# Kernel optimization log

Measured on AMD Instinct MI355X. Metric: run time of the kernel, lower is better.

## Reference

```python
import jax, jax.numpy as jnp
import numpy as np

B, S, D, H = 2, 2048, 1024, 16
HW = D // H  # head width = 64
MASK_FILL = -100000000.0


def setup_inputs() -> dict:
    key0 = jax.random.key(0)
    ks = jax.random.split(key0, 12)
    inp = {
        "query": jax.random.normal(ks[0], (B, S, D), jnp.float32),
        "key": jax.random.normal(ks[1], (B, S, D), jnp.float32),
        "value": jax.random.normal(ks[2], (B, S, D), jnp.float32),
        # bool mask, True masks; broadcasts over batch and heads
        "mask": jax.random.randint(ks[3], (S, S), 0, 2).astype(jnp.bool_),
        # per-head projection kernels: (heads, head_width, d_in)
        "Wq": jax.random.normal(ks[4], (H, HW, D), jnp.float32) * 0.02,
        "bq": jnp.zeros((H, HW), jnp.float32),
        "Wk": jax.random.normal(ks[5], (H, HW, D), jnp.float32) * 0.02,
        "bk": jnp.zeros((H, HW), jnp.float32),
        "Wv": jax.random.normal(ks[6], (H, HW, D), jnp.float32) * 0.02,
        "bv": jnp.zeros((H, HW), jnp.float32),
        # collapse projector: contracts (heads, head_width) -> d_output
        "Wo": jax.random.normal(ks[7], (D, H, HW), jnp.float32) * 0.02,
        "bo": jnp.zeros((D,), jnp.float32),
    }
    return inp


def reference(query, key, value, mask, Wq, bq, Wk, bk, Wv, bv, Wo, bo):
    # head projections -> (b, h, s, w)
    q = jnp.einsum("bsd,hwd->bhsw", query, Wq) + bq[:, None, :]
    k = jnp.einsum("btd,hwd->bhtw", key, Wk) + bk[:, None, :]
    v = jnp.einsum("btd,hwd->bhtw", value, Wv) + bv[:, None, :]
    # unscaled logits, masked_fill, softmax (matches original exactly)
    logits = jnp.einsum("bhsw,bhtw->bhst", q, k)
    logits = jnp.where(mask, MASK_FILL, logits)
    score = jax.nn.softmax(logits, axis=-1)
    # NOTE: original divides AV output by sqrt(head_width) AFTER softmax
    attn = jnp.einsum("bhst,bhtw->bhsw", score, v) / jnp.sqrt(jnp.float32(HW))
    # collapse heads -> (b, s, d_output)
    out = jnp.einsum("bhsw,ohw->bso", attn, Wo) + bo
    return out
```

## Files before the change

### kernel.cpp

```cpp
#include <hip/hip_runtime.h>
#include <math.h>

#define S_LEN   2048
#define D_MODEL 1024
#define N_HEADS 16
#define HEAD_W  64
#define BATCH   2
#define MROWS   (BATCH * S_LEN)
#define MASK_FILL -100000000.0f
#define LOG2E 1.4426950408889634f

typedef __attribute__((ext_vector_type(8))) short bf16x8;
typedef __attribute__((ext_vector_type(4))) float f32x4;
typedef unsigned short u16;
typedef unsigned int   u32;
typedef unsigned long long u64;

__device__ __forceinline__ u16 f2bf(float f) {
    u32 u = __float_as_uint(f);
    return (u16)((u + 0x7fffu + ((u >> 16) & 1u)) >> 16);
}

__device__ __forceinline__ void gld_lds16(const void* gp, void* lp) {
    __builtin_amdgcn_global_load_lds(
        (const __attribute__((address_space(1))) u32*)gp,
        (__attribute__((address_space(3))) u32*)lp, 16, 0, 0);
}

__global__ __launch_bounds__(256) void mask_bits_kernel(
    const unsigned char* __restrict__ mask, u64* __restrict__ bits) {
    __shared__ int isByte;
    if (threadIdx.x == 0) isByte = 0;
    __syncthreads();
    const int e0 = blockIdx.x * 2048;
    const uint2 v = ((const uint2*)(mask + e0))[threadIdx.x];
    if (((v.x | v.y) & 0xFFFFFF00u) != 0u) isByte = 1;
    __syncthreads();
    const int ib = isByte;
    const int* mi = (const int*)mask;
#pragma unroll
    for (int j = 0; j < 8; ++j) {
        const int e = e0 + j * 256 + threadIdx.x;
        const bool m = ib ? (mask[e] != 0) : (mi[e] != 0);
        const u64 bl = __ballot(m);
        if ((e & 63) == 0) bits[e >> 6] = bl;
    }
}

struct CvtJobs {
    const float* src[7];
    u16* dst[7];
    int n[7];
};
__global__ void cvt_bf16_kernel(CvtJobs j) {
    const int t = blockIdx.y;
    const float* s = j.src[t];
    u16* d = j.dst[t];
    const int n = j.n[t];
    int i = (blockIdx.x * 256 + threadIdx.x) * 4;
    if (i < n) {
        float4 v = *(const float4*)(s + i);
        ushort4 o;
        o.x = f2bf(v.x); o.y = f2bf(v.y); o.z = f2bf(v.z); o.w = f2bf(v.w);
        *(ushort4*)(d + i) = o;
    }
}

__device__ __forceinline__ void gemm_core_bf16(const u16* __restrict__ A,
                                               const u16* __restrict__ Bt,
                                               int m0, int n0, f32x4 acc[4][4]) {
    __shared__ u16 As[2][4096];
    __shared__ u16 Bs[2][4096];
    const int tid = threadIdx.x;
    const int wv = tid >> 6, ln = tid & 63;
    const int lane16 = ln & 15, quad = ln >> 4;
    const int wr = (wv >> 1) * 64, wc = (wv & 1) * 64;
    const u16* A0 = A + (size_t)(m0 + ln) * D_MODEL + wv * 8;
    const u16* A1 = A + (size_t)(m0 + 64 + ln) * D_MODEL + wv * 8;
    const u16* B0 = Bt + (size_t)(n0 + ln) * D_MODEL + wv * 8;
    const u16* B1 = Bt + (size_t)(n0 + 64 + ln) * D_MODEL + wv * 8;

    gld_lds16(A0, &As[0][wv * 1024]);
    gld_lds16(A1, &As[0][wv * 1024 + 512]);
    gld_lds16(B0, &Bs[0][wv * 1024]);
    gld_lds16(B1, &Bs[0][wv * 1024 + 512]);

    for (int kt = 0; kt < D_MODEL / 32; ++kt) {
        const int buf = kt & 1;
        __syncthreads();
        if (kt < D_MODEL / 32 - 1) {
            const int ko = (kt + 1) * 32;
            gld_lds16(A0 + ko, &As[buf ^ 1][wv * 1024]);
            gld_lds16(A1 + ko, &As[buf ^ 1][wv * 1024 + 512]);
            gld_lds16(B0 + ko, &Bs[buf ^ 1][wv * 1024]);
            gld_lds16(B1 + ko, &Bs[buf ^ 1][wv * 1024 + 512]);
        }
        bf16x8 af[4], bfv[4];
#pragma unroll
        for (int mt = 0; mt < 4; ++mt)
            af[mt] = *(const bf16x8*)&As[buf][quad * 1024 + (wr + mt * 16 + lane16) * 8];
#pragma unroll
        for (int nt = 0; nt < 4; ++nt)
            bfv[nt] = *(const bf16x8*)&Bs[buf][quad * 1024 + (wc + nt * 16 + lane16) * 8];
#pragma unroll
        for (int mt = 0; mt < 4; ++mt)
#pragma unroll
            for (int nt = 0; nt < 4; ++nt)
                acc[mt][nt] = __builtin_amdgcn_mfma_f32_16x16x32_bf16(
                    af[mt], bfv[nt], acc[mt][nt], 0, 0, 0);
    }
}

__global__ __launch_bounds__(256, 2) void qkv_gemm_kernel(
    const u16* __restrict__ xq, const u16* __restrict__ xk, const u16* __restrict__ xv,
    const u16* __restrict__ wq, const u16* __restrict__ wk, const u16* __restrict__ wv,
    const float* __restrict__ bq, const float* __restrict__ bk, const float* __restrict__ bv,
    u16* __restrict__ qb, u16* __restrict__ kb, u16* __restrict__ vtmp) {
    const u16* A; const u16* Bt; const float* bias; u16* outp;
    const int z = blockIdx.z;
    if (z == 0)      { A = xq; Bt = wq; bias = bq; outp = qb; }
    else if (z == 1) { A = xk; Bt = wk; bias = bk; outp = kb; }
    else             { A = xv; Bt = wv; bias = bv; outp = vtmp; }
    f32x4 acc[4][4] = {};
    const int m0 = blockIdx.y * 128, n0 = blockIdx.x * 128;
    gemm_core_bf16(A, Bt, m0, n0, acc);

    const int tid = threadIdx.x;
    const int wvi = tid >> 6, ln = tid & 63;
    const int lane16 = ln & 15, quad = ln >> 4;
    const int wr = (wvi >> 1) * 64, wc = (wvi & 1) * 64;
    const float scale = (z == 0) ? LOG2E : 1.0f;
#pragma unroll
    for (int nt = 0; nt < 4; ++nt) {
        const int n = n0 + wc + nt * 16 + lane16;
        const float bb = bias[n];
        const int h = n >> 6, w = n & 63;
#pragma unroll
        for (int mt = 0; mt < 4; ++mt)
#pragma unroll
            for (int r = 0; r < 4; ++r) {
                const int m = m0 + wr + mt * 16 + quad * 4 + r;
                const int bidx = m >> 11, s = m & 2047;
                outp[((size_t)((bidx * N_HEADS + h) * S_LEN + s)) * HEAD_W + w] =
                    f2bf((acc[mt][nt][r] + bb) * scale);
            }
    }
}

__global__ __launch_bounds__(256) void vtrans_kernel(
    const u16* __restrict__ vtmp, u16* __restrict__ vbt) {
    __shared__ u16 T[64][72];
    const int tid = threadIdx.x;
    const int bh = blockIdx.y;
    const int s0 = blockIdx.x * 64;
    const int row = tid >> 2, seg = (tid & 3) * 16;
    const u16* src = vtmp + ((size_t)bh * S_LEN + s0 + row) * HEAD_W + seg;
    uint4 a = *(const uint4*)src;
    uint4 b2 = *(const uint4*)(src + 8);
    u16 tmp[16];
    *(uint4*)tmp = a; *(uint4*)(tmp + 8) = b2;
#pragma unroll
    for (int j = 0; j < 16; ++j) T[seg + j][row] = tmp[j];
    __syncthreads();
    u16* dst = vbt + ((size_t)bh * HEAD_W + row) * S_LEN + s0 + seg;
    *(uint4*)dst       = *(const uint4*)&T[row][seg];
    *(uint4*)(dst + 8) = *(const uint4*)&T[row][seg + 8];
}

__global__ __launch_bounds__(256, 2) void out_gemm_kernel(
    const u16* __restrict__ ab, const u16* __restrict__ wo,
    const float* __restrict__ bo, float* __restrict__ out) {
    f32x4 acc[4][4] = {};
    const int m0 = blockIdx.y * 128, n0 = blockIdx.x * 128;
    gemm_core_bf16(ab, wo, m0, n0, acc);
    const int tid = threadIdx.x;
    const int wvi = tid >> 6, ln = tid & 63;
    const int lane16 = ln & 15, quad = ln >> 4;
    const int wr = (wvi >> 1) * 64, wc = (wvi & 1) * 64;
#pragma unroll
    for (int nt = 0; nt < 4; ++nt) {
        const int n = n0 + wc + nt * 16 + lane16;
        const float bb = bo[n];
#pragma unroll
        for (int mt = 0; mt < 4; ++mt)
#pragma unroll
            for (int r = 0; r < 4; ++r) {
                const int m = m0 + wr + mt * 16 + quad * 4 + r;
                out[(size_t)m * D_MODEL + n] = acc[mt][nt][r] + bb;
            }
    }
}

__global__ __launch_bounds__(256, 2) void attn_kernel(
    const u16* __restrict__ qbuf, const u16* __restrict__ kbuf,
    const u16* __restrict__ vbt, const u64* __restrict__ mbits,
    float* __restrict__ Opart, float* __restrict__ lpart) {
    __shared__ u16 Ks[2][4096];
    __shared__ u16 Vt[2][4096];
    __shared__ u16 Ps[4][32 * 72];
    const int tid = threadIdx.x;
    const int wv = tid >> 6, ln = tid & 63;
    const int lane16 = ln & 15, quad = ln >> 4;
    const int s_blk = blockIdx.x * 128;
    const int h = blockIdx.y;
    const int b = blockIdx.z >> 1, hf = blockIdx.z & 1;
    const int c0 = hf * 16;
    const size_t hb = ((size_t)(b * N_HEADS + h)) * S_LEN * HEAD_W;
    const u16* Qg = qbuf + hb;
    const u16* Kg = kbuf + hb;
    const u16* Vg = vbt + hb;

    bf16x8 qa[2][2];
#pragma unroll
    for (int mt = 0; mt < 2; ++mt)
#pragma unroll
        for (int kk = 0; kk < 2; ++kk)
            qa[mt][kk] = *(const bf16x8*)(Qg +
                (size_t)(s_blk + wv * 32 + mt * 16 + lane16) * HEAD_W + kk * 32 + quad * 8);

    const size_t mrow0 = (size_t)(s_blk + wv * 32 + lane16) * 32;
    const size_t mrow1 = (size_t)(s_blk + wv * 32 + 16 + lane16) * 32;
    u64 mwCur0 = mbits[mrow0 + c0], mwCur1 = mbits[mrow1 + c0];
    u64 mwNx0 = 0, mwNx1 = 0;

    {
        const int t0g = c0 * 64;
        const int i0 = 2 * wv, i1 = 2 * wv + 1;
        gld_lds16(Kg + (size_t)(t0g + ln) * HEAD_W + i0 * 8, &Ks[0][i0 * 512]);
        gld_lds16(Kg + (size_t)(t0g + ln) * HEAD_W + i1 * 8, &Ks[0][i1 * 512]);
        gld_lds16(Vg + (size_t)ln * S_LEN + t0g + i0 * 8, &Vt[0][i0 * 512]);
        gld_lds16(Vg + (size_t)ln * S_LEN + t0g + i1 * 8, &Vt[0][i1 * 512]);
    }

    f32x4 oacc[2][4] = {};
    float lsum[2] = {0.0f, 0.0f};

    for (int ci = 0; ci < 16; ++ci) {
        const int c = c0 + ci;
        const int buf = ci & 1;
        __syncthreads();
        if (ci < 15) {
            const int t1 = (c + 1) * 64;
            const int i0 = 2 * wv, i1 = 2 * wv + 1;
            gld_lds16(Kg + (size_t)(t1 + ln) * HEAD_W + i0 * 8, &Ks[buf ^ 1][i0 * 512]);
            gld_lds16(Kg + (size_t)(t1 + ln) * HEAD_W + i1 * 8, &Ks[buf ^ 1][i1 * 512]);
            gld_lds16(Vg + (size_t)ln * S_LEN + t1 + i0 * 8, &Vt[buf ^ 1][i0 * 512]);
            gld_lds16(Vg + (size_t)ln * S_LEN + t1 + i1 * 8, &Vt[buf ^ 1][i1 * 512]);
            mwNx0 = mbits[mrow0 + c + 1];
            mwNx1 = mbits[mrow1 + c + 1];
        }

        f32x4 st[4][2] = {};
#pragma unroll
        for (int kk = 0; kk < 2; ++kk)
#pragma unroll
            for (int ntT = 0; ntT < 4; ++ntT) {
                bf16x8 kf = *(const bf16x8*)&Ks[buf][(kk * 4 + quad) * 512 + (ntT * 16 + lane16) * 8];
#pragma unroll
                for (int mt = 0; mt < 2; ++mt)
                    st[ntT][mt] = __builtin_amdgcn_mfma_f32_16x16x32_bf16(
                        kf, qa[mt][kk], st[ntT][mt], 0, 0, 0);
            }

#pragma unroll
        for (int mt = 0; mt < 2; ++mt) {
            const u64 mw = mt ? mwCur1 : mwCur0;
            float ls = 0.0f;
#pragma unroll
            for (int ntT = 0; ntT < 4; ++ntT) {
                const u32 nib = (u32)(mw >> (ntT * 16 + quad * 4)) & 15u;
                float p0 = exp2f(st[ntT][mt][0]); if (nib & 1u) p0 = 0.0f;
                float p1 = exp2f(st[ntT][mt][1]); if (nib & 2u) p1 = 0.0f;
                float p2 = exp2f(st[ntT][mt][2]); if (nib & 4u) p2 = 0.0f;
                float p3 = exp2f(st[ntT][mt][3]); if (nib & 8u) p3 = 0.0f;
                ls += (p0 + p1) + (p2 + p3);
                uint2 pk;
                pk.x = __builtin_amdgcn_perm(__float_as_uint(p1) + 0x8000u,
                                             __float_as_uint(p0) + 0x8000u, 0x07060302u);
                pk.y = __builtin_amdgcn_perm(__float_as_uint(p3) + 0x8000u,
                                             __float_as_uint(p2) + 0x8000u, 0x07060302u);
                *(uint2*)&Ps[wv][(mt * 16 + lane16) * 72 + ntT * 16 + quad * 4] = pk;
            }
            lsum[mt] += ls;
        }

        bf16x8 pf[2][2];
#pragma unroll
        for (int mt = 0; mt < 2; ++mt)
#pragma unroll
            for (int kk = 0; kk < 2; ++kk)
                pf[mt][kk] = *(const bf16x8*)&Ps[wv][(mt * 16 + lane16) * 72 + kk * 32 + quad * 8];
#pragma unroll
        for (int kk = 0; kk < 2; ++kk)
#pragma unroll
            for (int ntw = 0; ntw < 4; ++ntw) {
                bf16x8 vf = *(const bf16x8*)&Vt[buf][(kk * 4 + quad) * 512 + (ntw * 16 + lane16) * 8];
#pragma unroll
                for (int mt = 0; mt < 2; ++mt)
                    oacc[mt][ntw] = __builtin_amdgcn_mfma_f32_16x16x32_bf16(
                        pf[mt][kk], vf, oacc[mt][ntw], 0, 0, 0);
            }
        mwCur0 = mwNx0; mwCur1 = mwNx1;
    }

    float* OpB = Opart + ((size_t)(hf * 4096 + b * 2048)) * 1024;
#pragma unroll
    for (int mt = 0; mt < 2; ++mt) {
#pragma unroll
        for (int r = 0; r < 4; ++r) {
            const int s = s_blk + wv * 32 + mt * 16 + quad * 4 + r;
            float* dst = OpB + (size_t)s * 1024 + h * 64;
#pragma unroll
            for (int ntw = 0; ntw < 4; ++ntw)
                dst[ntw * 16 + lane16] = oacc[mt][ntw][r];
        }
        float lm = lsum[mt];
        lm += __shfl_xor(lm, 16);
        lm += __shfl_xor(lm, 32);
        if (quad == 0) {
            const int srow = s_blk + wv * 32 + mt * 16 + lane16;
            lpart[(size_t)(hf * 4096 + b * 2048 + srow) * 16 + h] = lm;
        }
    }
}

__global__ __launch_bounds__(256) void combine_kernel(
    const float* __restrict__ Op, const float* __restrict__ lp,
    u16* __restrict__ ab) {
    const int idx4 = blockIdx.x * 256 + threadIdx.x;
    const int row = idx4 >> 8;
    const int d = (idx4 & 255) * 4;
    const int h = d >> 6;
    const float l = lp[(size_t)row * 16 + h] + lp[(size_t)(4096 + row) * 16 + h];
    const float inv = 0.125f / l;
    float4 a = *(const float4*)(Op + (size_t)row * 1024 + d);
    float4 b = *(const float4*)(Op + (size_t)(4096 + row) * 1024 + d);
    ushort4 o;
    o.x = f2bf((a.x + b.x) * inv);
    o.y = f2bf((a.y + b.y) * inv);
    o.z = f2bf((a.z + b.z) * inv);
    o.w = f2bf((a.w + b.w) * inv);
    *(ushort4*)(ab + (size_t)row * 1024 + d) = o;
}

extern "C" void kernel_launch(void* const* d_in, const int* in_sizes, int n_in,
                              void* d_out, int out_size, void* d_ws, size_t ws_size,
                              hipStream_t stream) {
    const float* query = (const float*)d_in[0];
    const float* key   = (const float*)d_in[1];
    const float* value = (const float*)d_in[2];
    const void*  mask  = d_in[3];
    const float* Wq = (const float*)d_in[4];
    const float* bq = (const float*)d_in[5];
    const float* Wk = (const float*)d_in[6];
    const float* bk = (const float*)d_in[7];
    const float* Wv = (const float*)d_in[8];
    const float* bv = (const float*)d_in[9];
    const float* Wo = (const float*)d_in[10];
    const float* bo = (const float*)d_in[11];
    float* out = (float*)d_out;

    char* ws = (char*)d_ws;
    const size_t MB = 1024 * 1024;
    u64* bits = (u64*)ws;
    u16* wob  = (u16*)(ws + 1 * MB);
    u16* qb   = (u16*)(ws + 3 * MB);
    u16* kb   = (u16*)(ws + 11 * MB);
    u16* vbt  = (u16*)(ws + 19 * MB);
    char* uA = ws + 27 * MB;
    u16* xq   = (u16*)(uA);
    u16* xk   = (u16*)(uA + 8 * MB);
    u16* xv   = (u16*)(uA + 16 * MB);
    u16* wqb  = (u16*)(uA + 24 * MB);
    u16* wkb  = (u16*)(uA + 26 * MB);
    u16* wvb  = (u16*)(uA + 28 * MB);
    u16* vtmp = (u16*)(uA + 30 * MB);
    float* Opart = (float*)(uA);
    float* lpart = (float*)(uA + 32 * MB);
    u16* ab = qb;

    const size_t NACT = (size_t)MROWS * D_MODEL;
    const size_t NW   = (size_t)D_MODEL * D_MODEL;

    mask_bits_kernel<<<2048, 256, 0, stream>>>((const unsigned char*)mask, bits);

    CvtJobs j;
    j.src[0] = query; j.dst[0] = xq;  j.n[0] = (int)NACT;
    j.src[1] = key;   j.dst[1] = xk;  j.n[1] = (int)NACT;
    j.src[2] = value; j.dst[2] = xv;  j.n[2] = (int)NACT;
    j.src[3] = Wq;    j.dst[3] = wqb; j.n[3] = (int)NW;
    j.src[4] = Wk;    j.dst[4] = wkb; j.n[4] = (int)NW;
    j.src[5] = Wv;    j.dst[5] = wvb; j.n[5] = (int)NW;
    j.src[6] = Wo;    j.dst[6] = wob; j.n[6] = (int)NW;
    cvt_bf16_kernel<<<dim3(NACT / 1024, 7), 256, 0, stream>>>(j);

    qkv_gemm_kernel<<<dim3(D_MODEL / 128, MROWS / 128, 3), 256, 0, stream>>>(
        xq, xk, xv, wqb, wkb, wvb, bq, bk, bv, qb, kb, vtmp);
    vtrans_kernel<<<dim3(S_LEN / 64, BATCH * N_HEADS), 256, 0, stream>>>(vtmp, vbt);
    attn_kernel<<<dim3(S_LEN / 128, N_HEADS, BATCH * 2), 256, 0, stream>>>(
        qb, kb, vbt, bits, Opart, lpart);
    combine_kernel<<<4096, 256, 0, stream>>>(Opart, lpart, ab);
    out_gemm_kernel<<<dim3(D_MODEL / 128, MROWS / 128), 256, 0, stream>>>(
        ab, wob, bo, out);
}
```

Before: 313.8 us.

## Fuse mask-bit and bf16 conversion kernels, raise occupancy bounds, use intrinsic bf16 pack

```diff
diff --git a/kernel.cpp b/kernel.cpp
--- a/kernel.cpp
+++ b/kernel.cpp
@@ -1,4 +1,5 @@
 #include <hip/hip_runtime.h>
+#include <hip/hip_bf16.h>
 #include <math.h>
 
 #define S_LEN   2048
@@ -21,14 +22,41 @@
     return (u16)((u + 0x7fffu + ((u >> 16) & 1u)) >> 16);
 }
 
+__device__ __forceinline__ u32 pack_bf16x2(float lo, float hi) {
+    __hip_bfloat162 t = __float22bfloat162_rn(make_float2(lo, hi));
+    u32 r;
+    __builtin_memcpy(&r, &t, 4);
+    return r;
+}
+
 __device__ __forceinline__ void gld_lds16(const void* gp, void* lp) {
     __builtin_amdgcn_global_load_lds(
         (const __attribute__((address_space(1))) u32*)gp,
         (__attribute__((address_space(3))) u32*)lp, 16, 0, 0);
 }
 
-__global__ __launch_bounds__(256) void mask_bits_kernel(
-    const unsigned char* __restrict__ mask, u64* __restrict__ bits) {
+struct CvtJobs {
+    const float* src[7];
+    u16* dst[7];
+    int n[7];
+};
+__global__ __launch_bounds__(256) void prep_kernel(
+    CvtJobs j, const unsigned char* __restrict__ mask, u64* __restrict__ bits) {
+    const int t = blockIdx.y;
+    if (t < 7) {
+        const float* s = j.src[t];
+        u16* d = j.dst[t];
+        const int n = j.n[t];
+        int i = (blockIdx.x * 256 + threadIdx.x) * 4;
+        if (i < n) {
+            float4 v = *(const float4*)(s + i);
+            ushort4 o;
+            o.x = f2bf(v.x); o.y = f2bf(v.y); o.z = f2bf(v.z); o.w = f2bf(v.w);
+            *(ushort4*)(d + i) = o;
+        }
+        return;
+    }
+    if (blockIdx.x >= 2048) return;
     __shared__ int isByte;
     if (threadIdx.x == 0) isByte = 0;
     __syncthreads();
@@ -39,30 +67,11 @@
     const int ib = isByte;
     const int* mi = (const int*)mask;
 #pragma unroll
-    for (int j = 0; j < 8; ++j) {
-        const int e = e0 + j * 256 + threadIdx.x;
+    for (int jj = 0; jj < 8; ++jj) {
+        const int e = e0 + jj * 256 + threadIdx.x;
         const bool m = ib ? (mask[e] != 0) : (mi[e] != 0);
         const u64 bl = __ballot(m);
         if ((e & 63) == 0) bits[e >> 6] = bl;
-    }
-}
-
-struct CvtJobs {
-    const float* src[7];
-    u16* dst[7];
-    int n[7];
-};
-__global__ void cvt_bf16_kernel(CvtJobs j) {
-    const int t = blockIdx.y;
-    const float* s = j.src[t];
-    u16* d = j.dst[t];
-    const int n = j.n[t];
-    int i = (blockIdx.x * 256 + threadIdx.x) * 4;
-    if (i < n) {
-        float4 v = *(const float4*)(s + i);
-        ushort4 o;
-        o.x = f2bf(v.x); o.y = f2bf(v.y); o.z = f2bf(v.z); o.w = f2bf(v.w);
-        *(ushort4*)(d + i) = o;
     }
 }
 
@@ -111,7 +120,7 @@
     }
 }
 
-__global__ __launch_bounds__(256, 2) void qkv_gemm_kernel(
+__global__ __launch_bounds__(256, 4) void qkv_gemm_kernel(
     const u16* __restrict__ xq, const u16* __restrict__ xk, const u16* __restrict__ xv,
     const u16* __restrict__ wq, const u16* __restrict__ wk, const u16* __restrict__ wv,
     const float* __restrict__ bq, const float* __restrict__ bk, const float* __restrict__ bv,
@@ -167,7 +176,7 @@
     *(uint4*)(dst + 8) = *(const uint4*)&T[row][seg + 8];
 }
 
-__global__ __launch_bounds__(256, 2) void out_gemm_kernel(
+__global__ __launch_bounds__(256, 4) void out_gemm_kernel(
     const u16* __restrict__ ab, const u16* __restrict__ wo,
     const float* __restrict__ bo, float* __restrict__ out) {
     f32x4 acc[4][4] = {};
@@ -191,7 +200,7 @@
     }
 }
 
-__global__ __launch_bounds__(256, 2) void attn_kernel(
+__global__ __launch_bounds__(256, 3) void attn_kernel(
     const u16* __restrict__ qbuf, const u16* __restrict__ kbuf,
     const u16* __restrict__ vbt, const u64* __restrict__ mbits,
     float* __restrict__ Opart, float* __restrict__ lpart) {
@@ -265,7 +274,7 @@
 #pragma unroll
         for (int mt = 0; mt < 2; ++mt) {
             const u64 mw = mt ? mwCur1 : mwCur0;
-            float ls = 0.0f;
+            float ls0 = 0.0f, ls1 = 0.0f;
 #pragma unroll
             for (int ntT = 0; ntT < 4; ++ntT) {
                 const u32 nib = (u32)(mw >> (ntT * 16 + quad * 4)) & 15u;
@@ -273,15 +282,14 @@
                 float p1 = exp2f(st[ntT][mt][1]); if (nib & 2u) p1 = 0.0f;
                 float p2 = exp2f(st[ntT][mt][2]); if (nib & 4u) p2 = 0.0f;
                 float p3 = exp2f(st[ntT][mt][3]); if (nib & 8u) p3 = 0.0f;
-                ls += (p0 + p1) + (p2 + p3);
+                ls0 += p0 + p1;
+                ls1 += p2 + p3;
                 uint2 pk;
-                pk.x = __builtin_amdgcn_perm(__float_as_uint(p1) + 0x8000u,
-                                             __float_as_uint(p0) + 0x8000u, 0x07060302u);
-                pk.y = __builtin_amdgcn_perm(__float_as_uint(p3) + 0x8000u,
-                                             __float_as_uint(p2) + 0x8000u, 0x07060302u);
+                pk.x = pack_bf16x2(p0, p1);
+                pk.y = pack_bf16x2(p2, p3);
                 *(uint2*)&Ps[wv][(mt * 16 + lane16) * 72 + ntT * 16 + quad * 4] = pk;
             }
-            lsum[mt] += ls;
+            lsum[mt] += ls0 + ls1;
         }
 
         bf16x8 pf[2][2];
@@ -382,8 +390,6 @@
     const size_t NACT = (size_t)MROWS * D_MODEL;
     const size_t NW   = (size_t)D_MODEL * D_MODEL;
 
-    mask_bits_kernel<<<2048, 256, 0, stream>>>((const unsigned char*)mask, bits);
-
     CvtJobs j;
     j.src[0] = query; j.dst[0] = xq;  j.n[0] = (int)NACT;
     j.src[1] = key;   j.dst[1] = xk;  j.n[1] = (int)NACT;
@@ -392,7 +398,8 @@
     j.src[4] = Wk;    j.dst[4] = wkb; j.n[4] = (int)NW;
     j.src[5] = Wv;    j.dst[5] = wvb; j.n[5] = (int)NW;
     j.src[6] = Wo;    j.dst[6] = wob; j.n[6] = (int)NW;
-    cvt_bf16_kernel<<<dim3(NACT / 1024, 7), 256, 0, stream>>>(j);
+    prep_kernel<<<dim3(NACT / 1024, 8), 256, 0, stream>>>(
+        j, (const unsigned char*)mask, bits);
 
     qkv_gemm_kernel<<<dim3(D_MODEL / 128, MROWS / 128, 3), 256, 0, stream>>>(
         xq, xk, xv, wqb, wkb, wvb, bq, bk, bv, qb, kb, vtmp);
```

Result: no change. 313.3 us (-0.2%).
